# Performance work log

Measured on AMD Instinct MI355X. Metric: run time of the kernel, lower is better.

The kernel has to match this reference:

```python
import jax, jax.numpy as jnp
import numpy as np

GAMMA = 0.99
LMBDA = 0.95

B, T, TAIL = 2048, 1024, 8


def setup_inputs() -> dict:
    key = jax.random.key(0)
    k1, k2, k3, k4 = jax.random.split(key, 4)
    reward = jax.random.normal(k1, (B, T, TAIL), dtype=jnp.float32)
    terminated = jax.random.bernoulli(k2, 0.01, (B, T, TAIL))  # bool, sparse terminations
    value = jax.random.normal(k3, (B, T, TAIL), dtype=jnp.float32)
    next_value = jax.random.normal(k4, (B, T, TAIL), dtype=jnp.float32)
    return {"reward": reward, "terminated": terminated, "value": value, "next_value": next_value}


def reference(reward, terminated, value, next_value):
    # not_done: 1 - terminated (float)
    not_done = 1.0 - terminated.astype(reward.dtype)
    # delta_t = r_t + gamma * V(s_{t+1}) * not_done_t - V(s_t)   -- fully elementwise
    delta = reward + GAMMA * next_value * not_done - value  # [B, T, tail]
    # Backward-in-time recurrence: gae_t = delta_t + gamma*lambda*not_done_t*gae_{t+1}
    delta_t = jnp.moveaxis(delta, 1, 0)      # [T, B, tail]
    nd_t = jnp.moveaxis(not_done, 1, 0)      # [T, B, tail]

    def step(gae, x):
        d, nd = x
        gae = d + (GAMMA * LMBDA) * nd * gae
        return gae, gae

    init = jnp.zeros(delta_t.shape[1:], dtype=reward.dtype)
    _, adv_t = jax.lax.scan(step, init, (delta_t, nd_t), reverse=True)
    advantages = jnp.moveaxis(adv_t, 0, 1)   # [B, T, tail]
    returns = advantages + value
    return advantages, returns
```

## Files before the change

kernel.cpp:

```cpp
#include <hip/hip_runtime.h>

#define BB    2048
#define TT    1024
#define TAILN 8
#define NELEM (BB * TT * TAILN)
#define ROWE  (TT * TAILN)
#define NSTEP 20
#define WSK   4

typedef float f32x4 __attribute__((ext_vector_type(4)));

static __global__ __launch_bounds__(256)
void detect_kernel(const unsigned int* __restrict__ term, int* __restrict__ flag) {
    __shared__ int sflag;
    if (threadIdx.x == 0) sflag = 0;
    __syncthreads();
    int ev = 0;
    #pragma unroll
    for (int j = 0; j < 16; ++j) {
        unsigned w = term[threadIdx.x + 256u * j];
        if (w == 0x3F800000u) ev |= 2;
        else if (w > 1u)      ev |= 1;
    }
    if (ev) atomicOr(&sflag, ev);
    __syncthreads();
    if (threadIdx.x == 0) *flag = sflag;
}

template <int MODE>
__device__ __forceinline__ void gae_wave(
    const float* __restrict__ r, const void* __restrict__ term,
    const float* __restrict__ v, const float* __restrict__ nv,
    float* __restrict__ adv, float* __restrict__ ret,
    int b, int c, int lane)
{
    const int  hi   = (c + 1) * 512 + 128;
    const bool ctop = (c == 1);
    const unsigned eb = (unsigned)b * (unsigned)ROWE;
    const int th = lane & 1;
    const int tq = lane >> 1;

    float cx = 0.0f, cy = 0.0f, cz = 0.0f, cw = 0.0f;

    auto load = [&](int k, float4& R4, float4& V4, float4& N4, uint4& T4) {
        int t0 = hi - 32 * (k + 1);
        if (t0 > TT - 32) t0 = TT - 32;
        const unsigned i = eb + (unsigned)t0 * 8u + ((unsigned)lane << 2);
        R4 = *(const float4*)(r  + i);
        V4 = *(const float4*)(v  + i);
        N4 = *(const float4*)(nv + i);
        if (MODE == 1)
            T4.x = ((const unsigned*)term)[((eb + (unsigned)t0 * 8u) >> 2)
                                           + (unsigned)lane];
        else
            T4 = *(const uint4*)((const unsigned*)term + i);
    };

    auto step = [&](int kk, const float4& R4, const float4& V4,
                    const float4& N4, const uint4& T4) {
        float n0, n1, n2, n3;
        if (MODE == 1) {
            n0 = ( T4.x        & 0xFFu) ? 0.0f : 1.0f;
            n1 = ((T4.x >>  8) & 0xFFu) ? 0.0f : 1.0f;
            n2 = ((T4.x >> 16) & 0xFFu) ? 0.0f : 1.0f;
            n3 = ((T4.x >> 24) & 0xFFu) ? 0.0f : 1.0f;
        } else if (MODE == 2) {
            n0 = 1.0f - __uint_as_float(T4.x);
            n1 = 1.0f - __uint_as_float(T4.y);
            n2 = 1.0f - __uint_as_float(T4.z);
            n3 = 1.0f - __uint_as_float(T4.w);
        } else {
            n0 = T4.x ? 0.0f : 1.0f;  n1 = T4.y ? 0.0f : 1.0f;
            n2 = T4.z ? 0.0f : 1.0f;  n3 = T4.w ? 0.0f : 1.0f;
        }
        float A0 = 0.9405f * n0, B0 = fmaf(0.99f * n0, N4.x, R4.x) - V4.x;
        float A1 = 0.9405f * n1, B1 = fmaf(0.99f * n1, N4.y, R4.y) - V4.y;
        float A2 = 0.9405f * n2, B2 = fmaf(0.99f * n2, N4.z, R4.z) - V4.z;
        float A3 = 0.9405f * n3, B3 = fmaf(0.99f * n3, N4.w, R4.w) - V4.w;

        #pragma unroll
        for (int s = 1; s < 32; s <<= 1) {
            const int  src   = lane + 2 * s;
            const bool valid = (tq + s) < 32;
            float a, bb;
            a = __shfl(A0, src); bb = __shfl(B0, src);
            B0 = fmaf(A0, valid ? bb : 0.0f, B0); A0 *= valid ? a : 1.0f;
            a = __shfl(A1, src); bb = __shfl(B1, src);
            B1 = fmaf(A1, valid ? bb : 0.0f, B1); A1 *= valid ? a : 1.0f;
            a = __shfl(A2, src); bb = __shfl(B2, src);
            B2 = fmaf(A2, valid ? bb : 0.0f, B2); A2 *= valid ? a : 1.0f;
            a = __shfl(A3, src); bb = __shfl(B3, src);
            B3 = fmaf(A3, valid ? bb : 0.0f, B3); A3 *= valid ? a : 1.0f;
        }

        if (ctop && kk == WSK) { cx = 0.0f; cy = 0.0f; cz = 0.0f; cw = 0.0f; }

        const float g0 = fmaf(A0, cx, B0);
        const float g1 = fmaf(A1, cy, B1);
        const float g2 = fmaf(A2, cz, B2);
        const float g3 = fmaf(A3, cw, B3);

        if (kk >= WSK) {
            const int t0 = hi - 32 * (kk + 1);
            const unsigned o = eb + (unsigned)t0 * 8u + ((unsigned)lane << 2);
            f32x4 g4; g4[0] = g0;        g4[1] = g1;        g4[2] = g2;        g4[3] = g3;
            f32x4 rr; rr[0] = g0 + V4.x; rr[1] = g1 + V4.y; rr[2] = g2 + V4.z; rr[3] = g3 + V4.w;
            __builtin_nontemporal_store(g4, (f32x4*)(adv + o));
            __builtin_nontemporal_store(rr, (f32x4*)(ret + o));
        }
        cx = __shfl(g0, th); cy = __shfl(g1, th);
        cz = __shfl(g2, th); cw = __shfl(g3, th);
    };

    float4 rA, vA, nA; uint4 tA;
    float4 rB, vB, nB; uint4 tB;
    float4 rC, vC, nC; uint4 tC;
    load(0, rA, vA, nA, tA);
    load(1, rB, vB, nB, tB);
    load(2, rC, vC, nC, tC);

    #pragma unroll
    for (int k = 0; k < NSTEP; ++k) {
        if (k % 3 == 0) {
            step(k, rA, vA, nA, tA);
            if (k + 3 < NSTEP) load(k + 3, rA, vA, nA, tA);
        } else if (k % 3 == 1) {
            step(k, rB, vB, nB, tB);
            if (k + 3 < NSTEP) load(k + 3, rB, vB, nB, tB);
        } else {
            step(k, rC, vC, nC, tC);
            if (k + 3 < NSTEP) load(k + 3, rC, vC, nC, tC);
        }
    }
}

__global__ __launch_bounds__(256)
void gae_kernel(const float* __restrict__ r, const void* __restrict__ term,
                const float* __restrict__ v, const float* __restrict__ nv,
                float* __restrict__ adv, float* __restrict__ ret,
                const int* __restrict__ flag)
{
    const int w    = threadIdx.x >> 6;
    const int lane = threadIdx.x & 63;
    const int b    = blockIdx.x * 2 + (w >> 1);
    const int c    = w & 1;
    const int f = *flag;
    if (f & 1)      gae_wave<1>(r, term, v, nv, adv, ret, b, c, lane);
    else if (f & 2) gae_wave<2>(r, term, v, nv, adv, ret, b, c, lane);
    else            gae_wave<0>(r, term, v, nv, adv, ret, b, c, lane);
}

extern "C" void kernel_launch(void* const* d_in, const int* in_sizes, int n_in,
                              void* d_out, int out_size, void* d_ws, size_t ws_size,
                              hipStream_t stream) {
    const float* reward = (const float*)d_in[0];
    const void*  term   = d_in[1];
    const float* value  = (const float*)d_in[2];
    const float* nextv  = (const float*)d_in[3];
    float* adv  = (float*)d_out;
    float* ret  = adv + NELEM;
    int*   flag = (int*)d_ws;

    hipLaunchKernelGGL(detect_kernel, dim3(1), dim3(256), 0, stream,
                       (const unsigned int*)term, flag);
    hipLaunchKernelGGL(gae_kernel, dim3(BB / 2), dim3(256), 0, stream,
                       reward, term, value, nextv, adv, ret, flag);
}
```

Measured before the change: 81.86 us.

## Split waves by tail half instead of time chunk, dropping warm-up overlap

```diff
diff --git a/kernel.cpp b/kernel.cpp
--- a/kernel.cpp
+++ b/kernel.cpp
@@ -5,8 +5,7 @@
 #define TAILN 8
 #define NELEM (BB * TT * TAILN)
 #define ROWE  (TT * TAILN)
-#define NSTEP 20
-#define WSK   4
+#define NSTEP 16
 
 typedef float f32x4 __attribute__((ext_vector_type(4)));
 
@@ -32,56 +31,51 @@
     const float* __restrict__ r, const void* __restrict__ term,
     const float* __restrict__ v, const float* __restrict__ nv,
     float* __restrict__ adv, float* __restrict__ ret,
-    int b, int c, int lane)
+    int b, int th, int lane)
 {
-    const int  hi   = (c + 1) * 512 + 128;
-    const bool ctop = (c == 1);
     const unsigned eb = (unsigned)b * (unsigned)ROWE;
-    const int th = lane & 1;
-    const int tq = lane >> 1;
+    const unsigned lo = (unsigned)lane * 8u + (unsigned)th * 4u;
 
-    float cx = 0.0f, cy = 0.0f, cz = 0.0f, cw = 0.0f;
+    float c0 = 0.0f, c1 = 0.0f, c2 = 0.0f, c3 = 0.0f;
 
-    auto load = [&](int k, float4& R4, float4& V4, float4& N4, uint4& T4) {
-        int t0 = hi - 32 * (k + 1);
-        if (t0 > TT - 32) t0 = TT - 32;
-        const unsigned i = eb + (unsigned)t0 * 8u + ((unsigned)lane << 2);
-        R4 = *(const float4*)(r  + i);
-        V4 = *(const float4*)(v  + i);
-        N4 = *(const float4*)(nv + i);
-        if (MODE == 1)
-            T4.x = ((const unsigned*)term)[((eb + (unsigned)t0 * 8u) >> 2)
-                                           + (unsigned)lane];
-        else
-            T4 = *(const uint4*)((const unsigned*)term + i);
-    };
+    #pragma unroll 4
+    for (int k = 0; k < NSTEP; ++k) {
+        const int t0 = TT - 64 * (k + 1);
+        const unsigned base = eb + (unsigned)t0 * 8u;
+        const unsigned i = base + lo;
 
-    auto step = [&](int kk, const float4& R4, const float4& V4,
-                    const float4& N4, const uint4& T4) {
+        const float4 R4 = *(const float4*)(r  + i);
+        const float4 V4 = *(const float4*)(v  + i);
+        const float4 N4 = *(const float4*)(nv + i);
+
         float n0, n1, n2, n3;
         if (MODE == 1) {
-            n0 = ( T4.x        & 0xFFu) ? 0.0f : 1.0f;
-            n1 = ((T4.x >>  8) & 0xFFu) ? 0.0f : 1.0f;
-            n2 = ((T4.x >> 16) & 0xFFu) ? 0.0f : 1.0f;
-            n3 = ((T4.x >> 24) & 0xFFu) ? 0.0f : 1.0f;
+            const unsigned tw = *(const unsigned*)((const unsigned char*)term + i);
+            n0 = ( tw        & 0xFFu) ? 0.0f : 1.0f;
+            n1 = ((tw >>  8) & 0xFFu) ? 0.0f : 1.0f;
+            n2 = ((tw >> 16) & 0xFFu) ? 0.0f : 1.0f;
+            n3 = ((tw >> 24) & 0xFFu) ? 0.0f : 1.0f;
         } else if (MODE == 2) {
+            const uint4 T4 = *(const uint4*)((const unsigned*)term + i);
             n0 = 1.0f - __uint_as_float(T4.x);
             n1 = 1.0f - __uint_as_float(T4.y);
             n2 = 1.0f - __uint_as_float(T4.z);
             n3 = 1.0f - __uint_as_float(T4.w);
         } else {
+            const uint4 T4 = *(const uint4*)((const unsigned*)term + i);
             n0 = T4.x ? 0.0f : 1.0f;  n1 = T4.y ? 0.0f : 1.0f;
             n2 = T4.z ? 0.0f : 1.0f;  n3 = T4.w ? 0.0f : 1.0f;
         }
+
         float A0 = 0.9405f * n0, B0 = fmaf(0.99f * n0, N4.x, R4.x) - V4.x;
         float A1 = 0.9405f * n1, B1 = fmaf(0.99f * n1, N4.y, R4.y) - V4.y;
         float A2 = 0.9405f * n2, B2 = fmaf(0.99f * n2, N4.z, R4.z) - V4.z;
         float A3 = 0.9405f * n3, B3 = fmaf(0.99f * n3, N4.w, R4.w) - V4.w;
 
         #pragma unroll
-        for (int s = 1; s < 32; s <<= 1) {
-            const int  src   = lane + 2 * s;
-            const bool valid = (tq + s) < 32;
+        for (int s = 1; s < 64; s <<= 1) {
+            const int  src   = lane + s;
+            const bool valid = (lane + s) < 64;
             float a, bb;
             a = __shfl(A0, src); bb = __shfl(B0, src);
             B0 = fmaf(A0, valid ? bb : 0.0f, B0); A0 *= valid ? a : 1.0f;
@@ -93,44 +87,18 @@
             B3 = fmaf(A3, valid ? bb : 0.0f, B3); A3 *= valid ? a : 1.0f;
         }
 
-        if (ctop && kk == WSK) { cx = 0.0f; cy = 0.0f; cz = 0.0f; cw = 0.0f; }
+        const float g0 = fmaf(A0, c0, B0);
+        const float g1 = fmaf(A1, c1, B1);
+        const float g2 = fmaf(A2, c2, B2);
+        const float g3 = fmaf(A3, c3, B3);
 
-        const float g0 = fmaf(A0, cx, B0);
-        const float g1 = fmaf(A1, cy, B1);
-        const float g2 = fmaf(A2, cz, B2);
-        const float g3 = fmaf(A3, cw, B3);
+        f32x4 a4; a4[0] = g0;        a4[1] = g1;        a4[2] = g2;        a4[3] = g3;
+        f32x4 r4; r4[0] = g0 + V4.x; r4[1] = g1 + V4.y; r4[2] = g2 + V4.z; r4[3] = g3 + V4.w;
+        *(f32x4*)(adv + i) = a4;
+        *(f32x4*)(ret + i) = r4;
 
-        if (kk >= WSK) {
-            const int t0 = hi - 32 * (kk + 1);
-            const unsigned o = eb + (unsigned)t0 * 8u + ((unsigned)lane << 2);
-            f32x4 g4; g4[0] = g0;        g4[1] = g1;        g4[2] = g2;        g4[3] = g3;
-            f32x4 rr; rr[0] = g0 + V4.x; rr[1] = g1 + V4.y; rr[2] = g2 + V4.z; rr[3] = g3 + V4.w;
-            __builtin_nontemporal_store(g4, (f32x4*)(adv + o));
-            __builtin_nontemporal_store(rr, (f32x4*)(ret + o));
-        }
-        cx = __shfl(g0, th); cy = __shfl(g1, th);
-        cz = __shfl(g2, th); cw = __shfl(g3, th);
-    };
-
-    float4 rA, vA, nA; uint4 tA;
-    float4 rB, vB, nB; uint4 tB;
-    float4 rC, vC, nC; uint4 tC;
-    load(0, rA, vA, nA, tA);
-    load(1, rB, vB, nB, tB);
-    load(2, rC, vC, nC, tC);
-
-    #pragma unroll
-    for (int k = 0; k < NSTEP; ++k) {
-        if (k % 3 == 0) {
-            step(k, rA, vA, nA, tA);
-            if (k + 3 < NSTEP) load(k + 3, rA, vA, nA, tA);
-        } else if (k % 3 == 1) {
-            step(k, rB, vB, nB, tB);
-            if (k + 3 < NSTEP) load(k + 3, rB, vB, nB, tB);
-        } else {
-            step(k, rC, vC, nC, tC);
-            if (k + 3 < NSTEP) load(k + 3, rC, vC, nC, tC);
-        }
+        c0 = __shfl(g0, 0); c1 = __shfl(g1, 0);
+        c2 = __shfl(g2, 0); c3 = __shfl(g3, 0);
     }
 }
 
@@ -143,11 +111,11 @@
     const int w    = threadIdx.x >> 6;
     const int lane = threadIdx.x & 63;
     const int b    = blockIdx.x * 2 + (w >> 1);
-    const int c    = w & 1;
+    const int th   = w & 1;
     const int f = *flag;
-    if (f & 1)      gae_wave<1>(r, term, v, nv, adv, ret, b, c, lane);
-    else if (f & 2) gae_wave<2>(r, term, v, nv, adv, ret, b, c, lane);
-    else            gae_wave<0>(r, term, v, nv, adv, ret, b, c, lane);
+    if (f & 1)      gae_wave<1>(r, term, v, nv, adv, ret, b, th, lane);
+    else if (f & 2) gae_wave<2>(r, term, v, nv, adv, ret, b, th, lane);
+    else            gae_wave<0>(r, term, v, nv, adv, ret, b, th, lane);
 }
 
 extern "C" void kernel_launch(void* const* d_in, const int* in_sizes, int n_in,
```

New measurement: 98.70 us. 1.21x slower.
